# Performance work log

Hardware: AMD Instinct MI355X
Metric: run time of the kernel (lower is better)

Reference implementation:

```python
import jax, jax.numpy as jnp
import numpy as np

B, S, D = 4, 2048, 1024
H, HD = 16, 64
WINDOW = 256


def setup_inputs() -> dict:
    key = jax.random.key(0)
    ks = jax.random.split(key, 5)
    scale = 1.0 / np.sqrt(D)
    return {
        "hidden_states": jax.random.normal(ks[0], (B, S, D), dtype=jnp.float32),
        "Wq": jax.random.normal(ks[1], (D, D), dtype=jnp.float32) * scale,
        "Wk": jax.random.normal(ks[2], (D, D), dtype=jnp.float32) * scale,
        "Wv": jax.random.normal(ks[3], (D, D), dtype=jnp.float32) * scale,
        "Wo": jax.random.normal(ks[4], (D, D), dtype=jnp.float32) * scale,
        "bo": jnp.zeros((D,), dtype=jnp.float32),
    }


def reference(hidden_states, Wq, Wk, Wv, Wo, bo):
    # q/k/v projections (no bias), torch Linear: x @ W.T
    q = hidden_states @ Wq.T  # [B,S,D]
    k = hidden_states @ Wk.T
    v = hidden_states @ Wv.T

    def split_heads(t):  # [B,S,D] -> [B,H,S,HD]
        return t.reshape(B, S, H, HD).transpose(0, 2, 1, 3)

    q, k, v = split_heads(q), split_heads(k), split_heads(v)

    # NOTE: original code does NOT scale by 1/sqrt(head_dim)
    scores = jnp.einsum("bhqd,bhkd->bhqk", q.astype(jnp.float32), k.astype(jnp.float32))

    # local causal band mask: keep j <= i and i - j < WINDOW
    i = jnp.arange(S)[:, None]
    j = jnp.arange(S)[None, :]
    band = (j <= i) & (i - j < WINDOW)  # [S,S] bool
    mask_value = jnp.finfo(scores.dtype).min
    scores = jnp.where(band[None, None, :, :], scores, mask_value)

    attn = jax.nn.softmax(scores, axis=-1).astype(v.dtype)
    ctx = jnp.einsum("bhqk,bhkd->bhqd", attn, v)  # [B,H,S,HD]

    # merge heads -> [B,S,D]
    ctx = ctx.transpose(0, 2, 1, 3).reshape(B, S, D)
    out = ctx @ Wo.T + bo
    return out
```

## Files before the change

kernel.cpp:

```cpp
#include <hip/hip_runtime.h>
#include <hip/hip_bf16.h>
#include <cstdint>
#include <cstddef>

#define S_LEN   2048
#define BATCH   4
#define NHEAD   16
#define HDIM    64
#define DMODEL  1024
#define WIN     256
#define PQ      72

typedef __bf16 bf16x8 __attribute__((ext_vector_type(8)));
typedef float f32x4 __attribute__((ext_vector_type(4)));
typedef unsigned short u16x4 __attribute__((ext_vector_type(4)));
typedef unsigned short u16x8 __attribute__((ext_vector_type(8)));

__device__ __forceinline__ unsigned short f2bf(float x) {
  union { float f; unsigned u; } c; c.f = x;
  unsigned r = (c.u + 0x7fffu + ((c.u >> 16) & 1u)) >> 16;
  return (unsigned short)r;
}

__device__ __forceinline__ void gld_lds16(const void* g, void* l) {
  __builtin_amdgcn_global_load_lds(
      (__attribute__((address_space(1))) void*)g,
      (__attribute__((address_space(3))) void*)l, 16, 0, 0);
}

__global__ __launch_bounds__(256) void convert_kernel(
    const float* __restrict__ s0, const float* __restrict__ s1,
    const float* __restrict__ s2, const float* __restrict__ s3,
    const float* __restrict__ s4,
    unsigned short* __restrict__ d0, unsigned short* __restrict__ d1,
    unsigned short* __restrict__ d2, unsigned short* __restrict__ d3,
    unsigned short* __restrict__ d4) {
  const int z = blockIdx.y;
  const float* s; unsigned short* d; long n;
  if      (z == 0) { s = s0; d = d0; n = (long)8192 * 1024; }
  else if (z == 1) { s = s1; d = d1; n = (long)1024 * 1024; }
  else if (z == 2) { s = s2; d = d2; n = (long)1024 * 1024; }
  else if (z == 3) { s = s3; d = d3; n = (long)1024 * 1024; }
  else             { s = s4; d = d4; n = (long)1024 * 1024; }
  const long base = ((long)blockIdx.x * 256 + threadIdx.x) * 16;
  if (base >= n) return;
#pragma unroll
  for (int i = 0; i < 4; ++i) {
    const float4 f = *(const float4*)(s + base + i * 4);
    u16x4 ov;
    ov.x = f2bf(f.x); ov.y = f2bf(f.y); ov.z = f2bf(f.z); ov.w = f2bf(f.w);
    *(u16x4*)(d + base + i * 4) = ov;
  }
}

template <int MODE>
__device__ __forceinline__ void gemm_bt_core(
    const unsigned short* __restrict__ A, const unsigned short* __restrict__ B,
    void* __restrict__ C, const float* __restrict__ bias,
    int M, int N, int K,
    unsigned short* __restrict__ lsA, unsigned short* __restrict__ lsB) {
  const int m0 = blockIdx.x * 128;
  const int n0 = blockIdx.y * 128;
  const int tid  = threadIdx.x;
  const int wave = tid >> 6, lane = tid & 63;
  const int quad = lane >> 4, l16 = lane & 15;
  const int wm = wave >> 1, wn = wave & 1;

  f32x4 acc[4][4];
#pragma unroll
  for (int i = 0; i < 4; ++i)
#pragma unroll
    for (int j = 0; j < 4; ++j) acc[i][j] = f32x4{0.f, 0.f, 0.f, 0.f};

  const int trow   = tid >> 3;
  const int tchunk = tid & 7;
  const int swz_w  = (trow >> 1) & 7;
  const int scol   = ((tchunk ^ swz_w) << 3);
  const int swz_r  = (l16 >> 1) & 7;

  for (int k0 = 0; k0 < K; k0 += 64) {
    __syncthreads();
#pragma unroll
    for (int c = 0; c < 4; ++c) {
      const int row  = trow + 32 * c;
      const int flat = row * 64 + tchunk * 8;
      gld_lds16(A + (size_t)(m0 + row) * K + k0 + scol, lsA + flat);
      gld_lds16(B + (size_t)(n0 + row) * K + k0 + scol, lsB + flat);
    }
    __syncthreads();

#pragma unroll
    for (int s2 = 0; s2 < 2; ++s2) {
      bf16x8 af[4], bfr[4];
#pragma unroll
      for (int mi = 0; mi < 4; ++mi)
        af[mi] = *(const bf16x8*)(lsA + (wm * 64 + mi * 16 + l16) * 64 +
                                  (((s2 * 4 + quad) ^ swz_r) << 3));
#pragma unroll
      for (int ni = 0; ni < 4; ++ni)
        bfr[ni] = *(const bf16x8*)(lsB + (wn * 64 + ni * 16 + l16) * 64 +
                                   (((s2 * 4 + quad) ^ swz_r) << 3));
#pragma unroll
      for (int mi = 0; mi < 4; ++mi)
#pragma unroll
        for (int ni = 0; ni < 4; ++ni)
          acc[mi][ni] = __builtin_amdgcn_mfma_f32_16x16x32_bf16(
              af[mi], bfr[ni], acc[mi][ni], 0, 0, 0);
    }
  }

#pragma unroll
  for (int mi = 0; mi < 4; ++mi) {
    if (MODE == 2) {
      const int mB = m0 + wm * 64 + mi * 16 + quad * 4;
      const int bq = mB >> 11, s = mB & 2047;
#pragma unroll
      for (int ni = 0; ni < 4; ++ni) {
        const int n = n0 + wn * 64 + ni * 16 + l16;
        u16x4 w;
        w[0] = f2bf(acc[mi][ni][0]); w[1] = f2bf(acc[mi][ni][1]);
        w[2] = f2bf(acc[mi][ni][2]); w[3] = f2bf(acc[mi][ni][3]);
        *(u16x4*)((unsigned short*)C +
                  (((size_t)((bq << 4) | (n >> 6)) * 64 + (n & 63)) << 11) + s) = w;
      }
    } else {
#pragma unroll
      for (int r = 0; r < 4; ++r) {
        const int m = m0 + wm * 64 + mi * 16 + quad * 4 + r;
#pragma unroll
        for (int ni = 0; ni < 4; ++ni) {
          const int n = n0 + wn * 64 + ni * 16 + l16;
          const float vv = acc[mi][ni][r];
          if (MODE == 0) {
            ((unsigned short*)C)[(size_t)m * N + n] = f2bf(vv);
          } else {
            ((float*)C)[(size_t)m * N + n] = vv + bias[n];
          }
        }
      }
    }
  }
}

__global__ __launch_bounds__(256) void gemm_qkv_kernel(
    const unsigned short* __restrict__ A,
    const unsigned short* __restrict__ B0, const unsigned short* __restrict__ B1,
    const unsigned short* __restrict__ B2,
    unsigned short* __restrict__ C0, unsigned short* __restrict__ C1,
    unsigned short* __restrict__ Cv, int M, int N, int K) {
  __shared__ unsigned short lsA[128 * 64];
  __shared__ unsigned short lsB[128 * 64];
  if (blockIdx.z == 2) {
    gemm_bt_core<2>(A, B2, Cv, nullptr, M, N, K, lsA, lsB);
  } else {
    const unsigned short* B = blockIdx.z == 0 ? B0 : B1;
    unsigned short*       C = blockIdx.z == 0 ? C0 : C1;
    gemm_bt_core<0>(A, B, C, nullptr, M, N, K, lsA, lsB);
  }
}

__global__ __launch_bounds__(256) void gemm_out_kernel(
    const unsigned short* __restrict__ A, const unsigned short* __restrict__ B,
    float* __restrict__ C, const float* __restrict__ bias, int M, int N, int K) {
  __shared__ unsigned short lsA[128 * 64];
  __shared__ unsigned short lsB[128 * 64];
  gemm_bt_core<1>(A, B, C, bias, M, N, K, lsA, lsB);
}

__global__ __launch_bounds__(256) void attn_kernel(
    const unsigned short* __restrict__ q, const unsigned short* __restrict__ k,
    const unsigned short* __restrict__ vt, unsigned short* __restrict__ ctx) {
  const int bh = blockIdx.y;
  const int b = bh >> 4, h = bh & 15;
  const int i0 = blockIdx.x * 128;
  const int tid  = threadIdx.x;
  const int wave = tid >> 6, lane = tid & 63;
  const int quad = lane >> 4, l16 = lane & 15;

  __shared__ unsigned short lsQ[128 * PQ];
  __shared__ unsigned short lsK[64 * PQ];
  __shared__ unsigned short lsVp[64 * PQ];

  {
    const int r = tid >> 1, cb = (tid & 1) * 32;
    const unsigned short* src =
        q + ((size_t)(b * S_LEN + i0 + r) * DMODEL + h * HDIM + cb);
    *(u16x8*)(lsQ + r * PQ + cb)      = *(const u16x8*)src;
    *(u16x8*)(lsQ + r * PQ + cb + 8)  = *(const u16x8*)(src + 8);
    *(u16x8*)(lsQ + r * PQ + cb + 16) = *(const u16x8*)(src + 16);
    *(u16x8*)(lsQ + r * PQ + cb + 24) = *(const u16x8*)(src + 24);
  }

  const int rr = tid >> 2, cb = (tid & 3) * 16;
  const int jhi  = cb >> 4;
  const int vbase = (jhi >> 1) * 32 + (jhi & 1) * 4;

  const int jb0 = (i0 >= WIN) ? ((i0 - WIN + 1) >> 6) : 0;
  const int jb1 = (i0 + 127) >> 6;
  const int jbi = i0 >> 6;

  u16x8 pk0, pk1, pv0, pv1;
  {
    const int j0 = jb0 * 64;
    const unsigned short* ks =
        k + ((size_t)(b * S_LEN + j0 + rr) * DMODEL + h * HDIM + cb);
    pk0 = *(const u16x8*)ks;
    pk1 = *(const u16x8*)(ks + 8);
    const unsigned short* vs =
        vt + ((size_t)(bh * HDIM + rr) * S_LEN + j0 + cb);
    pv0 = *(const u16x8*)vs;
    pv1 = *(const u16x8*)(vs + 8);
  }

  __syncthreads();

  bf16x8 aq[2][2];
#pragma unroll
  for (int t = 0; t < 2; ++t)
#pragma unroll
    for (int s2 = 0; s2 < 2; ++s2)
      aq[t][s2] = *(const bf16x8*)(lsQ + (wave * 32 + t * 16 + l16) * PQ +
                                   s2 * 32 + quad * 8);

  float l_lane[2] = {0.f, 0.f};
  f32x4 o[2][4];
#pragma unroll
  for (int t = 0; t < 2; ++t)
#pragma unroll
    for (int nd = 0; nd < 4; ++nd) o[t][nd] = f32x4{0.f, 0.f, 0.f, 0.f};

  for (int jb = jb0; jb <= jb1; ++jb) {
    const int j0 = jb * 64;
    const bool needMask = !(jb == jbi - 1 || jb == jbi - 2);
    __syncthreads();
    {
      *(u16x8*)(lsK + rr * PQ + cb)     = pk0;
      *(u16x8*)(lsK + rr * PQ + cb + 8) = pk1;
      u16x4 w0, w1, w2, w3;
      w0[0]=pv0[0]; w0[1]=pv0[1]; w0[2]=pv0[2]; w0[3]=pv0[3];
      w1[0]=pv0[4]; w1[1]=pv0[5]; w1[2]=pv0[6]; w1[3]=pv0[7];
      w2[0]=pv1[0]; w2[1]=pv1[1]; w2[2]=pv1[2]; w2[3]=pv1[3];
      w3[0]=pv1[4]; w3[1]=pv1[5]; w3[2]=pv1[6]; w3[3]=pv1[7];
      *(u16x4*)(lsVp + rr * PQ + vbase)      = w0;
      *(u16x4*)(lsVp + rr * PQ + vbase + 8)  = w1;
      *(u16x4*)(lsVp + rr * PQ + vbase + 16) = w2;
      *(u16x4*)(lsVp + rr * PQ + vbase + 24) = w3;
    }
    __syncthreads();

    if (jb < jb1) {
      const int jn = j0 + 64;
      const unsigned short* ks =
          k + ((size_t)(b * S_LEN + jn + rr) * DMODEL + h * HDIM + cb);
      pk0 = *(const u16x8*)ks;
      pk1 = *(const u16x8*)(ks + 8);
      const unsigned short* vs =
          vt + ((size_t)(bh * HDIM + rr) * S_LEN + jn + cb);
      pv0 = *(const u16x8*)vs;
      pv1 = *(const u16x8*)(vs + 8);
    }

    f32x4 st[2][4];
#pragma unroll
    for (int t = 0; t < 2; ++t)
#pragma unroll
      for (int ni = 0; ni < 4; ++ni) st[t][ni] = f32x4{0.f, 0.f, 0.f, 0.f};
    __builtin_amdgcn_s_setprio(1);
#pragma unroll
    for (int s2 = 0; s2 < 2; ++s2) {
      bf16x8 bk[4];
#pragma unroll
      for (int ni = 0; ni < 4; ++ni)
        bk[ni] = *(const bf16x8*)(lsK + (ni * 16 + l16) * PQ + s2 * 32 + quad * 8);
#pragma unroll
      for (int t = 0; t < 2; ++t)
#pragma unroll
        for (int ni = 0; ni < 4; ++ni)
          st[t][ni] = __builtin_amdgcn_mfma_f32_16x16x32_bf16(
              bk[ni], aq[t][s2], st[t][ni], 0, 0, 0);
    }
    __builtin_amdgcn_s_setprio(0);

    bf16x8 ap[2][2];
#pragma unroll
    for (int t = 0; t < 2; ++t) {
      const int iq = i0 + wave * 32 + t * 16 + l16;
      if (needMask) {
#pragma unroll
        for (int ni = 0; ni < 4; ++ni)
#pragma unroll
          for (int r = 0; r < 4; ++r) {
            const int j = j0 + ni * 16 + quad * 4 + r;
            const bool ok = ((unsigned)(iq - j) < (unsigned)WIN);
            const float p = ok ? __expf(fminf(st[t][ni][r], 80.f)) : 0.f;
            st[t][ni][r] = p;
            l_lane[t] += p;
          }
      } else {
#pragma unroll
        for (int ni = 0; ni < 4; ++ni)
#pragma unroll
          for (int r = 0; r < 4; ++r) {
            const float p = __expf(fminf(st[t][ni][r], 80.f));
            st[t][ni][r] = p;
            l_lane[t] += p;
          }
      }
#pragma unroll
      for (int s2 = 0; s2 < 2; ++s2) {
        bf16x8 a;
#pragma unroll
        for (int r = 0; r < 4; ++r) {
          union { unsigned short u; __bf16 h; } c0, c1;
          c0.u = f2bf(st[t][2 * s2][r]);
          c1.u = f2bf(st[t][2 * s2 + 1][r]);
          a[r]     = c0.h;
          a[4 + r] = c1.h;
        }
        ap[t][s2] = a;
      }
    }

    __builtin_amdgcn_s_setprio(1);
#pragma unroll
    for (int s2 = 0; s2 < 2; ++s2) {
      bf16x8 bv[4];
#pragma unroll
      for (int nd = 0; nd < 4; ++nd)
        bv[nd] = *(const bf16x8*)(lsVp + (nd * 16 + l16) * PQ + s2 * 32 + quad * 8);
#pragma unroll
      for (int t = 0; t < 2; ++t)
#pragma unroll
        for (int nd = 0; nd < 4; ++nd)
          o[t][nd] = __builtin_amdgcn_mfma_f32_16x16x32_bf16(
              ap[t][s2], bv[nd], o[t][nd], 0, 0, 0);
    }
    __builtin_amdgcn_s_setprio(0);
  }

#pragma unroll
  for (int t = 0; t < 2; ++t) {
    float l = l_lane[t];
    l += __shfl_xor(l, 16, 64);
    l += __shfl_xor(l, 32, 64);
    const float invl = 1.f / l;
#pragma unroll
    for (int r = 0; r < 4; ++r) {
      const float inv = __shfl(invl, quad * 4 + r, 64);
      const int i = i0 + wave * 32 + t * 16 + quad * 4 + r;
#pragma unroll
      for (int nd = 0; nd < 4; ++nd)
        ctx[(size_t)(b * S_LEN + i) * DMODEL + h * HDIM + nd * 16 + l16] =
            f2bf(o[t][nd][r] * inv);
    }
  }
}

extern "C" void kernel_launch(void* const* d_in, const int* in_sizes, int n_in,
                              void* d_out, int out_size, void* d_ws, size_t ws_size,
                              hipStream_t stream) {
  const float* hs = (const float*)d_in[0];
  const float* Wq = (const float*)d_in[1];
  const float* Wk = (const float*)d_in[2];
  const float* Wv = (const float*)d_in[3];
  const float* Wo = (const float*)d_in[4];
  const float* bo = (const float*)d_in[5];
  float* out = (float*)d_out;

  const size_t MD = (size_t)8192 * 1024;
  const size_t DD = (size_t)1024 * 1024;
  unsigned short* hsb  = (unsigned short*)d_ws;
  unsigned short* wqb  = hsb + MD;
  unsigned short* wkb  = wqb + DD;
  unsigned short* wvb  = wkb + DD;
  unsigned short* wob  = wvb + DD;
  unsigned short* qb   = wob + DD;
  unsigned short* kb   = qb + MD;
  unsigned short* vtb  = kb + MD;
  unsigned short* ctxb = vtb + MD;

  convert_kernel<<<dim3(2048, 5), 256, 0, stream>>>(hs, Wq, Wk, Wv, Wo,
                                                    hsb, wqb, wkb, wvb, wob);
  gemm_qkv_kernel<<<dim3(64, 8, 3), 256, 0, stream>>>(hsb, wqb, wkb, wvb,
                                                      qb, kb, vtb, 8192, 1024, 1024);
  attn_kernel<<<dim3(16, 64), 256, 0, stream>>>(qb, kb, vtb, ctxb);
  gemm_out_kernel<<<dim3(64, 8), 256, 0, stream>>>(ctxb, wob, out, bo,
                                                   8192, 1024, 1024);
}
```

Measured before the change: 212.8 us.

## Rewrite QKV GEMM as triple-buffered 128x256 tile pipeline with 8 waves

Adds a new GEMM core for the QKV projection that uses 512-thread blocks computing 128x256 tiles. It triple-buffers the LDS stages, issuing asynchronous global-to-LDS loads two k-tiles ahead, split across the two half-steps of each iteration, and raises wave priority around the MFMA blocks. The aim is to hide global load latency behind matrix math and to raise data reuse per block. In exchange it uses 144KB of LDS per block and needs careful vmcnt accounting. The old core keeps only the plain and bias output modes for the output projection.

```diff
diff --git a/kernel.cpp b/kernel.cpp
--- a/kernel.cpp
+++ b/kernel.cpp
@@ -54,6 +54,180 @@
 }
 
 template <int MODE>
+__device__ __forceinline__ void gemm_pipe_core(
+    const unsigned short* __restrict__ A, const unsigned short* __restrict__ B,
+    void* __restrict__ C, const float* __restrict__ bias,
+    int M, int N, int K, unsigned short* __restrict__ ls) {
+  const int m0 = blockIdx.x * 128;
+  const int n0 = blockIdx.y * 256;
+  const int tid  = threadIdx.x;
+  const int lane = tid & 63;
+  const int wid  = tid >> 6;
+  const int quad = lane >> 4, l16 = lane & 15;
+  const int wm = wid >> 2, wn = wid & 3;
+
+  const int REG = 24576;
+
+  const int srow   = tid >> 3;
+  const int schunk = tid & 7;
+  const int scol   = ((schunk ^ ((tid >> 4) & 7)) << 3);
+
+  f32x4 acc[4][4];
+#pragma unroll
+  for (int i = 0; i < 4; ++i)
+#pragma unroll
+    for (int j = 0; j < 4; ++j) acc[i][j] = f32x4{0.f, 0.f, 0.f, 0.f};
+
+  const int NT = K >> 6;
+
+#pragma unroll
+  for (int tt = 0; tt < 2; ++tt) {
+    const int k0 = tt << 6;
+#pragma unroll
+    for (int q = 0; q < 2; ++q) {
+      const int row = srow + 64 * q;
+      gld_lds16(A + (size_t)(m0 + row) * K + k0 + scol,
+                ls + tt * REG + row * 64 + schunk * 8);
+    }
+#pragma unroll
+    for (int q = 0; q < 4; ++q) {
+      const int row = srow + 64 * q;
+      gld_lds16(B + (size_t)(n0 + row) * K + k0 + scol,
+                ls + tt * REG + 8192 + row * 64 + schunk * 8);
+    }
+  }
+  asm volatile("s_waitcnt vmcnt(6)" ::: "memory");
+  __builtin_amdgcn_s_barrier();
+  __builtin_amdgcn_sched_barrier(0);
+
+  for (int t = 0; t < NT; ++t) {
+    const int rt = t % 3;
+    const unsigned short* la = ls + rt * REG;
+    const unsigned short* lb = la + 8192;
+    const int ts = t + 2;
+    const int rs = ts % 3;
+    const bool doStage = ts < NT;
+    const int k0s = ts << 6;
+    unsigned short* da = ls + rs * REG;
+
+    {
+      bf16x8 af[4], bfr[4];
+#pragma unroll
+      for (int mi = 0; mi < 4; ++mi)
+        af[mi] = *(const bf16x8*)(la + (wm * 64 + mi * 16 + l16) * 64 +
+                                  ((quad ^ (l16 >> 1)) << 3));
+#pragma unroll
+      for (int ni = 0; ni < 4; ++ni)
+        bfr[ni] = *(const bf16x8*)(lb + (wn * 64 + ni * 16 + l16) * 64 +
+                                   ((quad ^ (l16 >> 1)) << 3));
+      if (doStage) {
+#pragma unroll
+        for (int q = 0; q < 2; ++q) {
+          const int row = srow + 64 * q;
+          gld_lds16(A + (size_t)(m0 + row) * K + k0s + scol,
+                    da + row * 64 + schunk * 8);
+        }
+        gld_lds16(B + (size_t)(n0 + srow) * K + k0s + scol,
+                  da + 8192 + srow * 64 + schunk * 8);
+      }
+      __builtin_amdgcn_s_setprio(1);
+#pragma unroll
+      for (int mi = 0; mi < 4; ++mi)
+#pragma unroll
+        for (int ni = 0; ni < 4; ++ni)
+          acc[mi][ni] = __builtin_amdgcn_mfma_f32_16x16x32_bf16(
+              af[mi], bfr[ni], acc[mi][ni], 0, 0, 0);
+      __builtin_amdgcn_s_setprio(0);
+    }
+    __builtin_amdgcn_s_barrier();
+    __builtin_amdgcn_sched_barrier(0);
+
+    {
+      bf16x8 af[4], bfr[4];
+#pragma unroll
+      for (int mi = 0; mi < 4; ++mi)
+        af[mi] = *(const bf16x8*)(la + (wm * 64 + mi * 16 + l16) * 64 +
+                                  (((4 + quad) ^ (l16 >> 1)) << 3));
+#pragma unroll
+      for (int ni = 0; ni < 4; ++ni)
+        bfr[ni] = *(const bf16x8*)(lb + (wn * 64 + ni * 16 + l16) * 64 +
+                                   (((4 + quad) ^ (l16 >> 1)) << 3));
+      if (doStage) {
+#pragma unroll
+        for (int q = 1; q < 4; ++q) {
+          const int row = srow + 64 * q;
+          gld_lds16(B + (size_t)(n0 + row) * K + k0s + scol,
+                    da + 8192 + row * 64 + schunk * 8);
+        }
+      }
+      __builtin_amdgcn_s_setprio(1);
+#pragma unroll
+      for (int mi = 0; mi < 4; ++mi)
+#pragma unroll
+        for (int ni = 0; ni < 4; ++ni)
+          acc[mi][ni] = __builtin_amdgcn_mfma_f32_16x16x32_bf16(
+              af[mi], bfr[ni], acc[mi][ni], 0, 0, 0);
+      __builtin_amdgcn_s_setprio(0);
+    }
+    if (t + 2 < NT) {
+      asm volatile("s_waitcnt vmcnt(6)" ::: "memory");
+    } else if (t + 1 < NT) {
+      asm volatile("s_waitcnt vmcnt(0)" ::: "memory");
+    }
+    __builtin_amdgcn_s_barrier();
+    __builtin_amdgcn_sched_barrier(0);
+  }
+
+#pragma unroll
+  for (int mi = 0; mi < 4; ++mi) {
+    if (MODE == 2) {
+      const int mB = m0 + wm * 64 + mi * 16 + quad * 4;
+      const int bq = mB >> 11, s = mB & 2047;
+#pragma unroll
+      for (int ni = 0; ni < 4; ++ni) {
+        const int n = n0 + wn * 64 + ni * 16 + l16;
+        u16x4 w;
+        w[0] = f2bf(acc[mi][ni][0]); w[1] = f2bf(acc[mi][ni][1]);
+        w[2] = f2bf(acc[mi][ni][2]); w[3] = f2bf(acc[mi][ni][3]);
+        *(u16x4*)((unsigned short*)C +
+                  (((size_t)((bq << 4) | (n >> 6)) * 64 + (n & 63)) << 11) + s) = w;
+      }
+    } else {
+#pragma unroll
+      for (int r = 0; r < 4; ++r) {
+        const int m = m0 + wm * 64 + mi * 16 + quad * 4 + r;
+#pragma unroll
+        for (int ni = 0; ni < 4; ++ni) {
+          const int n = n0 + wn * 64 + ni * 16 + l16;
+          const float vv = acc[mi][ni][r];
+          if (MODE == 0) {
+            ((unsigned short*)C)[(size_t)m * N + n] = f2bf(vv);
+          } else {
+            ((float*)C)[(size_t)m * N + n] = vv + bias[n];
+          }
+        }
+      }
+    }
+  }
+}
+
+__global__ __launch_bounds__(512, 2) void gemm_qkv_kernel(
+    const unsigned short* __restrict__ A,
+    const unsigned short* __restrict__ B0, const unsigned short* __restrict__ B1,
+    const unsigned short* __restrict__ B2,
+    unsigned short* __restrict__ C0, unsigned short* __restrict__ C1,
+    unsigned short* __restrict__ Cv, int M, int N, int K) {
+  __shared__ unsigned short ls[3 * 24576];
+  if (blockIdx.z == 2) {
+    gemm_pipe_core<2>(A, B2, Cv, nullptr, M, N, K, ls);
+  } else {
+    const unsigned short* B = blockIdx.z == 0 ? B0 : B1;
+    unsigned short*       C = blockIdx.z == 0 ? C0 : C1;
+    gemm_pipe_core<0>(A, B, C, nullptr, M, N, K, ls);
+  }
+}
+
+template <int MODE>
 __device__ __forceinline__ void gemm_bt_core(
     const unsigned short* __restrict__ A, const unsigned short* __restrict__ B,
     void* __restrict__ C, const float* __restrict__ bias,
@@ -111,51 +285,20 @@
 
 #pragma unroll
   for (int mi = 0; mi < 4; ++mi) {
-    if (MODE == 2) {
-      const int mB = m0 + wm * 64 + mi * 16 + quad * 4;
-      const int bq = mB >> 11, s = mB & 2047;
+#pragma unroll
+    for (int r = 0; r < 4; ++r) {
+      const int m = m0 + wm * 64 + mi * 16 + quad * 4 + r;
 #pragma unroll
       for (int ni = 0; ni < 4; ++ni) {
         const int n = n0 + wn * 64 + ni * 16 + l16;
-        u16x4 w;
-        w[0] = f2bf(acc[mi][ni][0]); w[1] = f2bf(acc[mi][ni][1]);
-        w[2] = f2bf(acc[mi][ni][2]); w[3] = f2bf(acc[mi][ni][3]);
-        *(u16x4*)((unsigned short*)C +
-                  (((size_t)((bq << 4) | (n >> 6)) * 64 + (n & 63)) << 11) + s) = w;
-      }
-    } else {
-#pragma unroll
-      for (int r = 0; r < 4; ++r) {
-        const int m = m0 + wm * 64 + mi * 16 + quad * 4 + r;
-#pragma unroll
-        for (int ni = 0; ni < 4; ++ni) {
-          const int n = n0 + wn * 64 + ni * 16 + l16;
-          const float vv = acc[mi][ni][r];
-          if (MODE == 0) {
-            ((unsigned short*)C)[(size_t)m * N + n] = f2bf(vv);
-          } else {
-            ((float*)C)[(size_t)m * N + n] = vv + bias[n];
-          }
+        const float vv = acc[mi][ni][r];
+        if (MODE == 0) {
+          ((unsigned short*)C)[(size_t)m * N + n] = f2bf(vv);
+        } else {
+          ((float*)C)[(size_t)m * N + n] = vv + bias[n];
         }
       }
     }
-  }
-}
-
-__global__ __launch_bounds__(256) void gemm_qkv_kernel(
-    const unsigned short* __restrict__ A,
-    const unsigned short* __restrict__ B0, const unsigned short* __restrict__ B1,
-    const unsigned short* __restrict__ B2,
-    unsigned short* __restrict__ C0, unsigned short* __restrict__ C1,
-    unsigned short* __restrict__ Cv, int M, int N, int K) {
-  __shared__ unsigned short lsA[128 * 64];
-  __shared__ unsigned short lsB[128 * 64];
-  if (blockIdx.z == 2) {
-    gemm_bt_core<2>(A, B2, Cv, nullptr, M, N, K, lsA, lsB);
-  } else {
-    const unsigned short* B = blockIdx.z == 0 ? B0 : B1;
-    unsigned short*       C = blockIdx.z == 0 ? C0 : C1;
-    gemm_bt_core<0>(A, B, C, nullptr, M, N, K, lsA, lsB);
   }
 }
 
@@ -381,7 +524,7 @@
 
   convert_kernel<<<dim3(2048, 5), 256, 0, stream>>>(hs, Wq, Wk, Wv, Wo,
                                                     hsb, wqb, wkb, wvb, wob);
-  gemm_qkv_kernel<<<dim3(64, 8, 3), 256, 0, stream>>>(hsb, wqb, wkb, wvb,
+  gemm_qkv_kernel<<<dim3(64, 4, 3), 512, 0, stream>>>(hsb, wqb, wkb, wvb,
                                                       qb, kb, vtb, 8192, 1024, 1024);
   attn_kernel<<<dim3(16, 64), 256, 0, stream>>>(qb, kb, vtb, ctxb);
   gemm_out_kernel<<<dim3(64, 8), 256, 0, stream>>>(ctxb, wob, out, bo,
```

Measured after the change: 215.9 us. No clear change (+1.5%).
